# Kernel optimization log

Measured on AMD Instinct MI355X. Metric: run time of the kernel, lower is better.

Reference implementation:

```python
import jax, jax.numpy as jnp
import numpy as np
import math

SCALE = 16
R_MAX = 4
ALPHA_DYN = 2.0


def _bilinear_down(x, Ho, Wo):
    # torch F.interpolate bilinear, align_corners=False, no antialias. x: [C,H,W]
    C, H, W = x.shape
    def coords(no, ni):
        src = jnp.maximum((jnp.arange(no, dtype=jnp.float32) + 0.5) * (ni / no) - 0.5, 0.0)
        i0 = jnp.floor(src).astype(jnp.int32)
        t = src - i0.astype(jnp.float32)
        return jnp.clip(i0, 0, ni - 1), jnp.clip(i0 + 1, 0, ni - 1), t
    r0, r1, tr = coords(Ho, H)
    c0, c1, tc = coords(Wo, W)
    x = x[:, r0, :] * (1.0 - tr)[None, :, None] + x[:, r1, :] * tr[None, :, None]
    x = x[:, :, c0] * (1.0 - tc)[None, None, :] + x[:, :, c1] * tc[None, None, :]
    return x


def _jbu(feat_lr, guide_hr, sx_raw, sy_raw, th_raw, sr_raw):
    B, C, Hl, Wl = feat_lr.shape
    Hh, Wh = guide_hr.shape[2], guide_hr.shape[3]

    # parameter transforms
    up = lambda p: jnp.repeat(jnp.repeat(p[0, 0], SCALE, axis=0), SCALE, axis=1)  # nearest, exact multiple
    sx = jnp.maximum(up(jnp.exp(sx_raw)), 1e-6)
    sy = jnp.maximum(up(jnp.exp(sy_raw)), 1e-6)
    th = up(math.pi * jnp.tanh(th_raw))
    sr = jnp.maximum(up(jnp.exp(sr_raw)), 1e-6)

    Yh, Xh = jnp.meshgrid(jnp.arange(Hh, dtype=jnp.float32), jnp.arange(Wh, dtype=jnp.float32), indexing='ij')
    uc = jnp.round((Yh + 0.5) / SCALE - 0.5).astype(jnp.int32)
    vc = jnp.round((Xh + 0.5) / SCALE - 0.5).astype(jnp.int32)

    R_map_sq = jnp.clip(ALPHA_DYN * jnp.maximum(sx, sy), 1.0, float(R_MAX)) ** 2
    guide_lr = _bilinear_down(guide_hr[0], Hl, Wl)  # [Cg,Hl,Wl]
    cos_t, sin_t = jnp.cos(th), jnp.sin(th)
    inv2sx2 = 1.0 / (2.0 * sx ** 2 + 1e-8)
    inv2sy2 = 1.0 / (2.0 * sy ** 2 + 1e-8)
    inv2sr2 = 1.0 / (2.0 * sr ** 2 + 1e-8)

    d = jnp.arange(-R_MAX, R_MAX + 1, dtype=jnp.int32)
    dys, dxs = jnp.meshgrid(d, d, indexing='ij')
    offs = jnp.stack([dys.ravel(), dxs.ravel()], axis=1)  # [(2R+1)^2, 2]

    g_hr = guide_hr[0]    # [Cg,Hh,Wh]
    f_lr = feat_lr[0]     # [C,Hl,Wl]

    def step(carry, off):
        num, den = carry
        dy, dx = off[0], off[1]
        ui = jnp.clip(uc + dy, 0, Hl - 1)  # [Hh,Wh] int32
        vi = jnp.clip(vc + dx, 0, Wl - 1)
        cur_dx = (Xh - (vi.astype(jnp.float32) * SCALE + (SCALE - 1) / 2.0)) / SCALE
        cur_dy = (Yh - (ui.astype(jnp.float32) * SCALE + (SCALE - 1) / 2.0)) / SCALE
        a = cur_dx * cos_t + cur_dy * sin_t
        b = -cur_dx * sin_t + cur_dy * cos_t
        g_lr_s = guide_lr[:, ui, vi]                       # [Cg,Hh,Wh] gather
        g_diff2 = jnp.sum((g_hr - g_lr_s) ** 2, axis=0)    # [Hh,Wh]
        log_w = -(a ** 2) * inv2sx2 - (b ** 2) * inv2sy2 - g_diff2 * inv2sr2
        mask = (dy * dy + dx * dx).astype(jnp.float32) <= R_map_sq
        w = jnp.exp(log_w) * mask.astype(jnp.float32)      # [Hh,Wh]
        f_s = f_lr[:, ui, vi]                              # [C,Hh,Wh] gather
        return (num + f_s * w[None], den + w), None

    num0 = jnp.zeros((C, Hh, Wh), jnp.float32)
    den0 = jnp.zeros((Hh, Wh), jnp.float32)
    (num, den), _ = jax.lax.scan(step, (num0, den0), offs)
    res = num / jnp.maximum(den, 1e-8)
    return res[None].astype(feat_lr.dtype)


def setup_inputs() -> dict:
    key = jax.random.key(0)
    k1, k2 = jax.random.split(key)
    feat_lr = jax.random.normal(k1, (1, 128, 32, 32), jnp.float32)
    guide_hr = jax.random.normal(k2, (1, 3, 512, 512), jnp.float32)
    sx_raw = jnp.full((1, 1, 32, 32), float(np.log(16.0)), jnp.float32)
    sy_raw = jnp.full((1, 1, 32, 32), float(np.log(16.0)), jnp.float32)
    th_raw = jnp.zeros((1, 1, 32, 32), jnp.float32)
    sr_raw = jnp.full((1, 1, 32, 32), float(np.log(0.12)), jnp.float32)
    return {"feat_lr": feat_lr, "guide_hr": guide_hr, "sx_raw": sx_raw,
            "sy_raw": sy_raw, "th_raw": th_raw, "sr_raw": sr_raw}


def reference(feat_lr, guide_hr, sx_raw, sy_raw, th_raw, sr_raw):
    return _jbu(feat_lr, guide_hr, sx_raw, sy_raw, th_raw, sr_raw)
```

## Files before the change

kernel.cpp:

```cpp
#include <hip/hip_runtime.h>
#include <math.h>

#define HH 512
#define WH 512
#define L2E 1.44269504f
#define PI_F 3.14159265358979323846f
#define FTK 72

typedef __attribute__((ext_vector_type(8))) short short8v;
typedef __attribute__((ext_vector_type(4))) float float4v;

__device__ const unsigned char ORD[64] = {
    0x44,
    0x34,0x43,0x45,0x54,
    0x33,0x35,0x53,0x55,
    0x24,0x42,0x46,0x64,
    0x23,0x25,0x32,0x36,0x52,0x56,0x63,0x65,
    0x22,0x26,0x62,0x66,
    0x14,0x41,0x47,0x74,
    0x13,0x15,0x31,0x37,0x51,0x57,0x73,0x75,
    0x12,0x16,0x21,0x27,0x61,0x67,0x72,0x76,
    0x04,0x40,0x48,0x84,
    0x03,0x05,0x30,0x38,0x50,0x58,0x83,0x85,
    0x11,0x17,0x71,0x77,
    0x02,0x06,0x20
};

__global__ __launch_bounds__(256, 4) void jbu_fused_kernel(
    const float* __restrict__ feat,
    const float* __restrict__ guide,
    const float* __restrict__ sx_raw,
    const float* __restrict__ sy_raw,
    const float* __restrict__ th_raw,
    const float* __restrict__ sr_raw,
    float* __restrict__ out)
{
    __shared__ __align__(16) unsigned short FT[128 * FTK];
    __shared__ float tabK[64], tabA[64], tabB[64];
    __shared__ float tabG0[64], tabG1[64], tabG2[64];
    __shared__ float hdr[6];

    const int tid = threadIdx.x;
    const int b   = blockIdx.x;
    const int cell = (b & 7) * 128 + (b >> 3);
    const int cu = cell >> 5, cv = cell & 31;

    if (tid < 64) {
        const int k = tid;
        const float sx  = fmaxf(__expf(sx_raw[cell]), 1e-6f);
        const float sy  = fmaxf(__expf(sy_raw[cell]), 1e-6f);
        const float tr  = fminf(fmaxf(th_raw[cell], -10.f), 10.f);
        const float e2t = __expf(2.0f * tr);
        const float thv = PI_F * ((e2t - 1.0f) / (e2t + 1.0f));
        const float sr  = fmaxf(__expf(sr_raw[cell]), 1e-6f);
        const float R   = fminf(fmaxf(2.0f * fmaxf(sx, sy), 1.0f), 4.0f);
        const float Rsq = R * R;
        float sth, cth;
        __sincosf(thv, &sth, &cth);
        const float i2sx = 1.0f / (2.0f * sx * sx + 1e-8f);
        const float i2sy = 1.0f / (2.0f * sy * sy + 1e-8f);
        const float i2sr = 1.0f / (2.0f * sr * sr + 1e-8f);
        if (k == 0) {
            hdr[0] = cth; hdr[1] = sth;
            hdr[2] = i2sx * L2E; hdr[3] = i2sy * L2E; hdr[4] = i2sr * L2E;
            hdr[5] = Rsq;
        }
        const int o  = ORD[k];
        const int dy = (o >> 4) - 4, dx = (o & 15) - 4;
        const int act = ((float)(dy * dy + dx * dx) <= Rsq);
        const int ui = min(max(cu + dy, 0), 31);
        const int vi = min(max(cv + dx, 0), 31);
        const int yg = ui * 16 + 7, xg = vi * 16 + 7;
        float gl[3];
        #pragma unroll
        for (int ch = 0; ch < 3; ++ch) {
            const float* g = guide + ch * (HH * WH);
            gl[ch] = 0.25f * (g[yg * WH + xg] + g[yg * WH + xg + 1]
                            + g[(yg + 1) * WH + xg] + g[(yg + 1) * WH + xg + 1]);
        }
        const float rk = (float)(vi - cv), tk = (float)(ui - cu);
        const float ak = rk * cth + tk * sth;
        const float bk = tk * cth - rk * sth;
        tabK[k]  = act ? -(ak * ak * i2sx + bk * bk * i2sy
                           + (gl[0]*gl[0] + gl[1]*gl[1] + gl[2]*gl[2]) * i2sr) * L2E
                       : -1e30f;
        tabA[k]  = 2.0f * ak * i2sx * L2E;
        tabB[k]  = 2.0f * bk * i2sy * L2E;
        tabG0[k] = 2.0f * gl[0] * i2sr * L2E;
        tabG1[k] = 2.0f * gl[1] * i2sr * L2E;
        tabG2[k] = 2.0f * gl[2] * i2sr * L2E;
    }

    const int wave = tid >> 6;
    const int lane = tid & 63;
    const int lg   = lane >> 4;
    const int pxx  = lane & 15;
    const int mtb  = wave * 4;

    float g0[4], g1[4], g2[4];
    #pragma unroll
    for (int mt = 0; mt < 4; ++mt) {
        const int y = cu * 16 + mtb + mt;
        const int o = y * WH + cv * 16 + pxx;
        g0[mt] = guide[o];
        g1[mt] = guide[HH * WH + o];
        g2[mt] = guide[2 * HH * WH + o];
    }

    {
        const int k  = tid & 63;
        const int cb = (tid >> 6) * 32;
        const int o  = ORD[k];
        const int ui = min(max(cu + (o >> 4) - 4, 0), 31);
        const int vi = min(max(cv + (o & 15) - 4, 0), 31);
        const float* fp = feat + ui * 32 + vi;
        #pragma unroll
        for (int j = 0; j < 32; ++j) {
            const float fv = fp[(cb + j) * 1024];
            const unsigned int bb = __float_as_uint(fv);
            FT[(cb + j) * FTK + k] =
                (unsigned short)((bb + 0x7FFFu + ((bb >> 16) & 1u)) >> 16);
        }
    }
    __syncthreads();

    const float cth = hdr[0], sth = hdr[1];
    const float i2sxl = hdr[2], i2syl = hdr[3], i2srl = hdr[4];
    const bool  use2 = hdr[5] >= 10.0f;
    const float qd = ((float)pxx - 7.5f) * 0.0625f;

    float a0[4], b0[4], P[4];
    #pragma unroll
    for (int mt = 0; mt < 4; ++mt) {
        const float pd = ((float)(mtb + mt) - 7.5f) * 0.0625f;
        a0[mt] = qd * cth + pd * sth;
        b0[mt] = pd * cth - qd * sth;
        P[mt]  = -(a0[mt]*a0[mt]*i2sxl + b0[mt]*b0[mt]*i2syl
                   + (g0[mt]*g0[mt] + g1[mt]*g1[mt] + g2[mt]*g2[mt]) * i2srl);
    }

    short8v Afrag[4][2];
    float den[4] = {0.f, 0.f, 0.f, 0.f};
    #pragma unroll
    for (int ks = 0; ks < 2; ++ks) {
        if (ks == 0 || use2) {
            float cK[8], cA[8], cB[8], cG0[8], cG1[8], cG2[8];
            #pragma unroll
            for (int i = 0; i < 8; ++i) {
                const int k = ks * 32 + lg * 8 + i;
                cK[i] = tabK[k];  cA[i] = tabA[k];  cB[i] = tabB[k];
                cG0[i] = tabG0[k]; cG1[i] = tabG1[k]; cG2[i] = tabG2[k];
            }
            #pragma unroll
            for (int mt = 0; mt < 4; ++mt) {
                short8v av;
                #pragma unroll
                for (int i = 0; i < 8; ++i) {
                    float lw = P[mt] + cK[i];
                    lw = fmaf(a0[mt], cA[i], lw);
                    lw = fmaf(b0[mt], cB[i], lw);
                    lw = fmaf(g0[mt], cG0[i], lw);
                    lw = fmaf(g1[mt], cG1[i], lw);
                    lw = fmaf(g2[mt], cG2[i], lw);
                    const float w = __builtin_amdgcn_exp2f(lw);
                    den[mt] += w;
                    const unsigned int bb = __float_as_uint(w);
                    av[i] = (short)((bb + 0x7FFFu + ((bb >> 16) & 1u)) >> 16);
                }
                Afrag[mt][ks] = av;
            }
        }
    }

    float invd[4][4];
    #pragma unroll
    for (int mt = 0; mt < 4; ++mt) {
        float d = den[mt];
        d += __shfl_xor(d, 16);
        d += __shfl_xor(d, 32);
        const float id = 1.0f / fmaxf(d, 1e-8f);
        #pragma unroll
        for (int r = 0; r < 4; ++r)
            invd[mt][r] = __shfl(id, lg * 4 + r);
    }

    #pragma unroll
    for (int nt = 0; nt < 8; ++nt) {
        const int ch = nt * 16 + pxx;
        short8v Bf0 = *(const short8v*)&FT[ch * FTK + lg * 8];
        short8v Bf1 = *(const short8v*)&FT[ch * FTK + 32 + lg * 8];
        const size_t chp = (size_t)ch * (HH * WH);
        #pragma unroll
        for (int mt = 0; mt < 4; ++mt) {
            float4v acc = {0.f, 0.f, 0.f, 0.f};
            acc = __builtin_amdgcn_mfma_f32_16x16x32_bf16(Afrag[mt][0], Bf0, acc, 0, 0, 0);
            if (use2)
                acc = __builtin_amdgcn_mfma_f32_16x16x32_bf16(Afrag[mt][1], Bf1, acc, 0, 0, 0);
            const int y = cu * 16 + mtb + mt;
            float4v res;
            res[0] = acc[0] * invd[mt][0];
            res[1] = acc[1] * invd[mt][1];
            res[2] = acc[2] * invd[mt][2];
            res[3] = acc[3] * invd[mt][3];
            *(float4v*)(out + chp + y * WH + cv * 16 + lg * 4) = res;
        }
    }
}

extern "C" void kernel_launch(void* const* d_in, const int* in_sizes, int n_in,
                              void* d_out, int out_size, void* d_ws, size_t ws_size,
                              hipStream_t stream) {
    const float* feat   = (const float*)d_in[0];
    const float* guide  = (const float*)d_in[1];
    const float* sx_raw = (const float*)d_in[2];
    const float* sy_raw = (const float*)d_in[3];
    const float* th_raw = (const float*)d_in[4];
    const float* sr_raw = (const float*)d_in[5];
    float* out = (float*)d_out;
    (void)d_ws; (void)ws_size;

    jbu_fused_kernel<<<1024, 256, 0, stream>>>(feat, guide, sx_raw, sy_raw,
                                               th_raw, sr_raw, out);
}
```

Measured before the change: 37.29 us.

## Process two horizontally adjacent low-res cells per block for wider output rows

Each block now handles a pair of neighboring low-resolution cells with 512 threads, each wave covering two output rows across both cells. Stores per row become 32 contiguous floats (128 bytes) instead of 16, which is meant to improve write coalescing on the output-bound store phase. The cost is a doubled shared-memory tile, a grid halved to 512 blocks, and use2 now being taken whenever either cell needs the second K-slice.

Measured after the change: 37.18 us. Within noise of the previous version (-0.3%).

```diff
diff --git a/kernel.cpp b/kernel.cpp
--- a/kernel.cpp
+++ b/kernel.cpp
@@ -26,7 +26,7 @@
     0x02,0x06,0x20
 };
 
-__global__ __launch_bounds__(256, 4) void jbu_fused_kernel(
+__global__ __launch_bounds__(512, 4) void jbu_pair_kernel(
     const float* __restrict__ feat,
     const float* __restrict__ guide,
     const float* __restrict__ sx_raw,
@@ -35,18 +35,22 @@
     const float* __restrict__ sr_raw,
     float* __restrict__ out)
 {
-    __shared__ __align__(16) unsigned short FT[128 * FTK];
-    __shared__ float tabK[64], tabA[64], tabB[64];
-    __shared__ float tabG0[64], tabG1[64], tabG2[64];
-    __shared__ float hdr[6];
+    __shared__ __align__(16) unsigned short FT[2 * 128 * FTK];
+    __shared__ float tabK[2][64], tabA[2][64], tabB[2][64];
+    __shared__ float tabG0[2][64], tabG1[2][64], tabG2[2][64];
+    __shared__ float hdr[2][8];
 
     const int tid = threadIdx.x;
     const int b   = blockIdx.x;
-    const int cell = (b & 7) * 128 + (b >> 3);
-    const int cu = cell >> 5, cv = cell & 31;
-
-    if (tid < 64) {
-        const int k = tid;
+    const int pair = (b & 7) * 64 + (b >> 3);
+    const int cu  = pair >> 4;
+    const int cv0 = (pair & 15) * 2;
+
+    if (tid < 128) {
+        const int c2 = tid >> 6;
+        const int k  = tid & 63;
+        const int cv = cv0 + c2;
+        const int cell = cu * 32 + cv;
         const float sx  = fmaxf(__expf(sx_raw[cell]), 1e-6f);
         const float sy  = fmaxf(__expf(sy_raw[cell]), 1e-6f);
         const float tr  = fminf(fmaxf(th_raw[cell], -10.f), 10.f);
@@ -61,9 +65,9 @@
         const float i2sy = 1.0f / (2.0f * sy * sy + 1e-8f);
         const float i2sr = 1.0f / (2.0f * sr * sr + 1e-8f);
         if (k == 0) {
-            hdr[0] = cth; hdr[1] = sth;
-            hdr[2] = i2sx * L2E; hdr[3] = i2sy * L2E; hdr[4] = i2sr * L2E;
-            hdr[5] = Rsq;
+            hdr[c2][0] = cth; hdr[c2][1] = sth;
+            hdr[c2][2] = i2sx * L2E; hdr[c2][3] = i2sy * L2E; hdr[c2][4] = i2sr * L2E;
+            hdr[c2][5] = Rsq;
         }
         const int o  = ORD[k];
         const int dy = (o >> 4) - 4, dx = (o & 15) - 4;
@@ -81,128 +85,154 @@
         const float rk = (float)(vi - cv), tk = (float)(ui - cu);
         const float ak = rk * cth + tk * sth;
         const float bk = tk * cth - rk * sth;
-        tabK[k]  = act ? -(ak * ak * i2sx + bk * bk * i2sy
-                           + (gl[0]*gl[0] + gl[1]*gl[1] + gl[2]*gl[2]) * i2sr) * L2E
-                       : -1e30f;
-        tabA[k]  = 2.0f * ak * i2sx * L2E;
-        tabB[k]  = 2.0f * bk * i2sy * L2E;
-        tabG0[k] = 2.0f * gl[0] * i2sr * L2E;
-        tabG1[k] = 2.0f * gl[1] * i2sr * L2E;
-        tabG2[k] = 2.0f * gl[2] * i2sr * L2E;
+        tabK[c2][k]  = act ? -(ak * ak * i2sx + bk * bk * i2sy
+                               + (gl[0]*gl[0] + gl[1]*gl[1] + gl[2]*gl[2]) * i2sr) * L2E
+                           : -1e30f;
+        tabA[c2][k]  = 2.0f * ak * i2sx * L2E;
+        tabB[c2][k]  = 2.0f * bk * i2sy * L2E;
+        tabG0[c2][k] = 2.0f * gl[0] * i2sr * L2E;
+        tabG1[c2][k] = 2.0f * gl[1] * i2sr * L2E;
+        tabG2[c2][k] = 2.0f * gl[2] * i2sr * L2E;
     }
 
     const int wave = tid >> 6;
     const int lane = tid & 63;
     const int lg   = lane >> 4;
     const int pxx  = lane & 15;
-    const int mtb  = wave * 4;
-
-    float g0[4], g1[4], g2[4];
-    #pragma unroll
-    for (int mt = 0; mt < 4; ++mt) {
+    const int mtb  = wave * 2;
+
+    float g0[2][2], g1[2][2], g2[2][2];
+    #pragma unroll
+    for (int mt = 0; mt < 2; ++mt) {
         const int y = cu * 16 + mtb + mt;
-        const int o = y * WH + cv * 16 + pxx;
-        g0[mt] = guide[o];
-        g1[mt] = guide[HH * WH + o];
-        g2[mt] = guide[2 * HH * WH + o];
+        #pragma unroll
+        for (int c2 = 0; c2 < 2; ++c2) {
+            const int o = y * WH + (cv0 + c2) * 16 + pxx;
+            g0[mt][c2] = guide[o];
+            g1[mt][c2] = guide[HH * WH + o];
+            g2[mt][c2] = guide[2 * HH * WH + o];
+        }
     }
 
     {
         const int k  = tid & 63;
-        const int cb = (tid >> 6) * 32;
+        const int c2 = (tid >> 6) & 1;
+        const int cb = (tid >> 7) * 32;
         const int o  = ORD[k];
         const int ui = min(max(cu + (o >> 4) - 4, 0), 31);
-        const int vi = min(max(cv + (o & 15) - 4, 0), 31);
+        const int vi = min(max(cv0 + c2 + (o & 15) - 4, 0), 31);
         const float* fp = feat + ui * 32 + vi;
+        unsigned short* ft = &FT[(c2 * 128) * FTK + k];
         #pragma unroll
         for (int j = 0; j < 32; ++j) {
             const float fv = fp[(cb + j) * 1024];
             const unsigned int bb = __float_as_uint(fv);
-            FT[(cb + j) * FTK + k] =
+            ft[(cb + j) * FTK] =
                 (unsigned short)((bb + 0x7FFFu + ((bb >> 16) & 1u)) >> 16);
         }
     }
     __syncthreads();
 
-    const float cth = hdr[0], sth = hdr[1];
-    const float i2sxl = hdr[2], i2syl = hdr[3], i2srl = hdr[4];
-    const bool  use2 = hdr[5] >= 10.0f;
+    const bool use2 = (hdr[0][5] >= 10.0f) || (hdr[1][5] >= 10.0f);
     const float qd = ((float)pxx - 7.5f) * 0.0625f;
 
-    float a0[4], b0[4], P[4];
-    #pragma unroll
-    for (int mt = 0; mt < 4; ++mt) {
-        const float pd = ((float)(mtb + mt) - 7.5f) * 0.0625f;
-        a0[mt] = qd * cth + pd * sth;
-        b0[mt] = pd * cth - qd * sth;
-        P[mt]  = -(a0[mt]*a0[mt]*i2sxl + b0[mt]*b0[mt]*i2syl
-                   + (g0[mt]*g0[mt] + g1[mt]*g1[mt] + g2[mt]*g2[mt]) * i2srl);
-    }
-
-    short8v Afrag[4][2];
-    float den[4] = {0.f, 0.f, 0.f, 0.f};
+    float a0[2][2], b0[2][2], P[2][2];
+    #pragma unroll
+    for (int c2 = 0; c2 < 2; ++c2) {
+        const float cth = hdr[c2][0], sth = hdr[c2][1];
+        const float i2sxl = hdr[c2][2], i2syl = hdr[c2][3], i2srl = hdr[c2][4];
+        #pragma unroll
+        for (int mt = 0; mt < 2; ++mt) {
+            const float pd = ((float)(mtb + mt) - 7.5f) * 0.0625f;
+            a0[mt][c2] = qd * cth + pd * sth;
+            b0[mt][c2] = pd * cth - qd * sth;
+            P[mt][c2]  = -(a0[mt][c2]*a0[mt][c2]*i2sxl + b0[mt][c2]*b0[mt][c2]*i2syl
+                           + (g0[mt][c2]*g0[mt][c2] + g1[mt][c2]*g1[mt][c2]
+                              + g2[mt][c2]*g2[mt][c2]) * i2srl);
+        }
+    }
+
+    short8v Afrag[2][2][2];
+    float den[2][2] = {{0.f, 0.f}, {0.f, 0.f}};
     #pragma unroll
     for (int ks = 0; ks < 2; ++ks) {
         if (ks == 0 || use2) {
-            float cK[8], cA[8], cB[8], cG0[8], cG1[8], cG2[8];
             #pragma unroll
-            for (int i = 0; i < 8; ++i) {
-                const int k = ks * 32 + lg * 8 + i;
-                cK[i] = tabK[k];  cA[i] = tabA[k];  cB[i] = tabB[k];
-                cG0[i] = tabG0[k]; cG1[i] = tabG1[k]; cG2[i] = tabG2[k];
-            }
-            #pragma unroll
-            for (int mt = 0; mt < 4; ++mt) {
-                short8v av;
+            for (int c2 = 0; c2 < 2; ++c2) {
+                float cK[8], cA[8], cB[8], cG0[8], cG1[8], cG2[8];
                 #pragma unroll
                 for (int i = 0; i < 8; ++i) {
-                    float lw = P[mt] + cK[i];
-                    lw = fmaf(a0[mt], cA[i], lw);
-                    lw = fmaf(b0[mt], cB[i], lw);
-                    lw = fmaf(g0[mt], cG0[i], lw);
-                    lw = fmaf(g1[mt], cG1[i], lw);
-                    lw = fmaf(g2[mt], cG2[i], lw);
-                    const float w = __builtin_amdgcn_exp2f(lw);
-                    den[mt] += w;
-                    const unsigned int bb = __float_as_uint(w);
-                    av[i] = (short)((bb + 0x7FFFu + ((bb >> 16) & 1u)) >> 16);
+                    const int k = ks * 32 + lg * 8 + i;
+                    cK[i] = tabK[c2][k];  cA[i] = tabA[c2][k];  cB[i] = tabB[c2][k];
+                    cG0[i] = tabG0[c2][k]; cG1[i] = tabG1[c2][k]; cG2[i] = tabG2[c2][k];
                 }
-                Afrag[mt][ks] = av;
+                #pragma unroll
+                for (int mt = 0; mt < 2; ++mt) {
+                    short8v av;
+                    #pragma unroll
+                    for (int i = 0; i < 8; ++i) {
+                        float lw = P[mt][c2] + cK[i];
+                        lw = fmaf(a0[mt][c2], cA[i], lw);
+                        lw = fmaf(b0[mt][c2], cB[i], lw);
+                        lw = fmaf(g0[mt][c2], cG0[i], lw);
+                        lw = fmaf(g1[mt][c2], cG1[i], lw);
+                        lw = fmaf(g2[mt][c2], cG2[i], lw);
+                        const float w = __builtin_amdgcn_exp2f(lw);
+                        den[mt][c2] += w;
+                        const unsigned int bb = __float_as_uint(w);
+                        av[i] = (short)((bb + 0x7FFFu + ((bb >> 16) & 1u)) >> 16);
+                    }
+                    Afrag[mt][c2][ks] = av;
+                }
             }
         }
     }
 
-    float invd[4][4];
-    #pragma unroll
-    for (int mt = 0; mt < 4; ++mt) {
-        float d = den[mt];
-        d += __shfl_xor(d, 16);
-        d += __shfl_xor(d, 32);
-        const float id = 1.0f / fmaxf(d, 1e-8f);
-        #pragma unroll
-        for (int r = 0; r < 4; ++r)
-            invd[mt][r] = __shfl(id, lg * 4 + r);
+    float invd[2][2][4];
+    #pragma unroll
+    for (int mt = 0; mt < 2; ++mt) {
+        #pragma unroll
+        for (int c2 = 0; c2 < 2; ++c2) {
+            float d = den[mt][c2];
+            d += __shfl_xor(d, 16);
+            d += __shfl_xor(d, 32);
+            const float id = 1.0f / fmaxf(d, 1e-8f);
+            #pragma unroll
+            for (int r = 0; r < 4; ++r)
+                invd[mt][c2][r] = __shfl(id, lg * 4 + r);
+        }
     }
 
     #pragma unroll
     for (int nt = 0; nt < 8; ++nt) {
         const int ch = nt * 16 + pxx;
-        short8v Bf0 = *(const short8v*)&FT[ch * FTK + lg * 8];
-        short8v Bf1 = *(const short8v*)&FT[ch * FTK + 32 + lg * 8];
+        short8v Bf0[2], Bf1[2];
+        #pragma unroll
+        for (int c2 = 0; c2 < 2; ++c2) {
+            Bf0[c2] = *(const short8v*)&FT[(c2 * 128 + ch) * FTK + lg * 8];
+            Bf1[c2] = *(const short8v*)&FT[(c2 * 128 + ch) * FTK + 32 + lg * 8];
+        }
         const size_t chp = (size_t)ch * (HH * WH);
         #pragma unroll
-        for (int mt = 0; mt < 4; ++mt) {
-            float4v acc = {0.f, 0.f, 0.f, 0.f};
-            acc = __builtin_amdgcn_mfma_f32_16x16x32_bf16(Afrag[mt][0], Bf0, acc, 0, 0, 0);
-            if (use2)
-                acc = __builtin_amdgcn_mfma_f32_16x16x32_bf16(Afrag[mt][1], Bf1, acc, 0, 0, 0);
+        for (int mt = 0; mt < 2; ++mt) {
             const int y = cu * 16 + mtb + mt;
-            float4v res;
-            res[0] = acc[0] * invd[mt][0];
-            res[1] = acc[1] * invd[mt][1];
-            res[2] = acc[2] * invd[mt][2];
-            res[3] = acc[3] * invd[mt][3];
-            *(float4v*)(out + chp + y * WH + cv * 16 + lg * 4) = res;
+            float* rowp = out + chp + y * WH + cv0 * 16;
+            float4v res[2];
+            #pragma unroll
+            for (int c2 = 0; c2 < 2; ++c2) {
+                float4v acc = {0.f, 0.f, 0.f, 0.f};
+                acc = __builtin_amdgcn_mfma_f32_16x16x32_bf16(
+                    Afrag[mt][c2][0], Bf0[c2], acc, 0, 0, 0);
+                if (use2)
+                    acc = __builtin_amdgcn_mfma_f32_16x16x32_bf16(
+                        Afrag[mt][c2][1], Bf1[c2], acc, 0, 0, 0);
+                res[c2][0] = acc[0] * invd[mt][c2][0];
+                res[c2][1] = acc[1] * invd[mt][c2][1];
+                res[c2][2] = acc[2] * invd[mt][c2][2];
+                res[c2][3] = acc[3] * invd[mt][c2][3];
+            }
+            *(float4v*)(rowp + lg * 4)      = res[0];
+            *(float4v*)(rowp + 16 + lg * 4) = res[1];
         }
     }
 }
@@ -219,6 +249,6 @@
     float* out = (float*)d_out;
     (void)d_ws; (void)ws_size;
 
-    jbu_fused_kernel<<<1024, 256, 0, stream>>>(feat, guide, sx_raw, sy_raw,
-                                               th_raw, sr_raw, out);
+    jbu_pair_kernel<<<512, 512, 0, stream>>>(feat, guide, sx_raw, sy_raw,
+                                             th_raw, sr_raw, out);
 }
```
